# Optimization experiments

Measured on AMD Instinct MI355X. Metric: run time of the kernel, lower is better.

## Reference

```python
import jax, jax.numpy as jnp
import numpy as np

D = 1024
H = 16
HD = D // H


def setup_inputs() -> dict:
    key = jax.random.key(0)
    ks = jax.random.split(key, 9)
    s = 1.0 / np.sqrt(D)
    return {
        "x": jax.random.normal(ks[0], (2, 2048, D), dtype=jnp.float32),
        "Wq": jax.random.normal(ks[1], (D, D), dtype=jnp.float32) * s,
        "bq": jax.random.normal(ks[2], (D,), dtype=jnp.float32) * s,
        "Wk": jax.random.normal(ks[3], (D, D), dtype=jnp.float32) * s,
        "bk": jax.random.normal(ks[4], (D,), dtype=jnp.float32) * s,
        "Wv": jax.random.normal(ks[5], (D, D), dtype=jnp.float32) * s,
        "bv": jax.random.normal(ks[6], (D,), dtype=jnp.float32) * s,
        "Wo": jax.random.normal(ks[7], (D, D), dtype=jnp.float32) * s,
        "bo": jax.random.normal(ks[8], (D,), dtype=jnp.float32) * s,
    }


def reference(x, Wq, bq, Wk, bk, Wv, bv, Wo, bo):
    B, S, _ = x.shape
    # Linear projections (torch Linear: y = x @ W.T + b)
    q = x @ Wq.T + bq
    k = x @ Wk.T + bk
    v = x @ Wv.T + bv
    # split heads: [B, S, H, HD] -> [B, H, S, HD]
    q = q.reshape(B, S, H, HD).transpose(0, 2, 1, 3)
    k = k.reshape(B, S, H, HD).transpose(0, 2, 1, 3)
    v = v.reshape(B, S, H, HD).transpose(0, 2, 1, 3)
    scale = 1.0 / jnp.sqrt(jnp.float32(HD))
    scores = jnp.einsum("bhqd,bhkd->bhqk", q, k) * scale  # [B,H,S,S]
    attn = jax.nn.softmax(scores, axis=-1)
    ctx = jnp.einsum("bhqk,bhkd->bhqd", attn, v)  # [B,H,S,HD]
    ctx = ctx.transpose(0, 2, 1, 3).reshape(B, S, D)
    out = ctx @ Wo.T + bo
    return out, attn
```

## Files before the change

### kernel.cpp

```cpp
#include <hip/hip_runtime.h>

#define S_LEN 2048
#define NH 16
#define HDIM 64
#define DMODEL 1024
#define NTOK 4096

typedef __attribute__((ext_vector_type(8))) short bf16x8;
typedef __attribute__((ext_vector_type(4))) float f32x4;

__device__ __forceinline__ unsigned short f2bf(float f) {
  union { float f; unsigned int u; } a; a.f = f;
  unsigned int u = a.u;
  u += 0x7FFFu + ((u >> 16) & 1u);
  return (unsigned short)(u >> 16);
}

__device__ __forceinline__ void gld_lds16(const unsigned short* g, unsigned short* l) {
  auto gp = (const __attribute__((address_space(1))) unsigned short*)(g);
  auto lp = (__attribute__((address_space(3))) unsigned short*)(l);
  __builtin_amdgcn_global_load_lds(gp, lp, 16, 0, 0);
}

__global__ __launch_bounds__(256) void cvt_kernel(const float* __restrict__ s,
                                                  unsigned short* __restrict__ d, int n) {
  int i = (blockIdx.x * 256 + threadIdx.x) * 4;
  if (i >= n) return;
  float4 v = *(const float4*)(s + i);
  ushort4 o;
  o.x = f2bf(v.x); o.y = f2bf(v.y); o.z = f2bf(v.z); o.w = f2bf(v.w);
  *(ushort4*)(d + i) = o;
}

__device__ __forceinline__ void gemm_core_128(
    const unsigned short* __restrict__ A, const unsigned short* __restrict__ B,
    unsigned short* Al, unsigned short* Bl, int m0, int n0, int tid, f32x4 acc[4][4])
{
  const int lane = tid & 63;
  const int wm = ((tid >> 6) >> 1) * 64;
  const int wn = ((tid >> 6) & 1) * 64;
  const int l15 = lane & 15, quad = lane >> 4;
  const int row0 = tid >> 2, c8 = (tid & 3) * 8;
  for (int kk = 0; kk < DMODEL; kk += 32) {
    gld_lds16(A + (size_t)(m0 + row0) * DMODEL + kk + c8,      Al + tid * 8);
    gld_lds16(A + (size_t)(m0 + 64 + row0) * DMODEL + kk + c8, Al + (256 + tid) * 8);
    gld_lds16(B + (size_t)(n0 + row0) * DMODEL + kk + c8,      Bl + tid * 8);
    gld_lds16(B + (size_t)(n0 + 64 + row0) * DMODEL + kk + c8, Bl + (256 + tid) * 8);
    __syncthreads();
    bf16x8 af[4], bfr[4];
#pragma unroll
    for (int i = 0; i < 4; i++) {
      af[i]  = *(const bf16x8*)(Al + (wm + i * 16 + l15) * 32 + quad * 8);
      bfr[i] = *(const bf16x8*)(Bl + (wn + i * 16 + l15) * 32 + quad * 8);
    }
#pragma unroll
    for (int i = 0; i < 4; i++)
#pragma unroll
      for (int j = 0; j < 4; j++)
        acc[i][j] = __builtin_amdgcn_mfma_f32_16x16x32_bf16(af[i], bfr[j], acc[i][j], 0, 0, 0);
    __syncthreads();
  }
}

__global__ __launch_bounds__(256) void gemm_qkv(
    const unsigned short* __restrict__ xb,
    const unsigned short* __restrict__ wq, const unsigned short* __restrict__ wk,
    const unsigned short* __restrict__ wv,
    const float* __restrict__ bq, const float* __restrict__ bk, const float* __restrict__ bv,
    unsigned short* __restrict__ q_ws, unsigned short* __restrict__ k_ws,
    unsigned short* __restrict__ vT_ws)
{
  __shared__ unsigned short Al[128 * 32];
  __shared__ unsigned short Bl[128 * 32];
  const int which = blockIdx.z;
  const unsigned short* W = which == 0 ? wq : (which == 1 ? wk : wv);
  const float* bias = which == 0 ? bq : (which == 1 ? bk : bv);
  const int m0 = blockIdx.y * 128, n0 = blockIdx.x * 128;
  const int tid = threadIdx.x, lane = tid & 63;
  const int wm = ((tid >> 6) >> 1) * 64, wn = ((tid >> 6) & 1) * 64;
  const int l15 = lane & 15, quad = lane >> 4;
  f32x4 acc[4][4] = {};
  gemm_core_128(xb, W, Al, Bl, m0, n0, tid, acc);
  const float scale = (which == 0) ? 0.125f : 1.0f;
  unsigned short* qk_dst = (which == 0) ? q_ws : k_ws;
#pragma unroll
  for (int j = 0; j < 4; j++) {
    const int n = n0 + wn + j * 16 + l15;
    const float bb = bias[n];
    const int h = n >> 6, d = n & 63;
#pragma unroll
    for (int i = 0; i < 4; i++)
#pragma unroll
      for (int r = 0; r < 4; r++) {
        const int m = m0 + wm + i * 16 + quad * 4 + r;
        const int b = m >> 11, s = m & 2047;
        const unsigned short o = f2bf((acc[i][j][r] + bb) * scale);
        if (which == 2)
          vT_ws[((size_t)(b * NH + h) * HDIM + d) * S_LEN + s] = o;
        else
          qk_dst[((size_t)(b * NH + h) * S_LEN + s) * HDIM + d] = o;
      }
  }
}

__global__ __launch_bounds__(256, 8) void attn_fused(
    const unsigned short* __restrict__ q_ws, const unsigned short* __restrict__ k_ws,
    const unsigned short* __restrict__ vT_ws,
    float* __restrict__ attn_out, unsigned short* __restrict__ ctx_ws)
{
  __shared__ __align__(16) unsigned short p_lds[4][16 * 72];
  __shared__ float ls[4][16];
  const int tid = threadIdx.x, lane = tid & 63, w = tid >> 6;
  const int l15 = lane & 15, quad = lane >> 4;
  const int rowg = w >> 1, khalf = w & 1;
  const int bh = blockIdx.x >> 6, qt = blockIdx.x & 63;
  const int qr0 = qt * 32 + rowg * 16;
  const int kc0 = khalf * 1024;

  const unsigned short* qp = q_ws + ((size_t)bh * S_LEN + qr0 + l15) * HDIM + quad * 8;
  bf16x8 aq0 = *(const bf16x8*)qp;
  bf16x8 aq1 = *(const bf16x8*)(qp + 32);

  const unsigned short* kbh = k_ws + (size_t)bh * S_LEN * HDIM;
  const unsigned short* vbh = vT_ws + (size_t)bh * HDIM * S_LEN;

  float lsum = 0.f;
  for (int kc = kc0; kc < kc0 + 1024; kc += 64) {
#pragma unroll
    for (int t = 0; t < 4; t++) {
      const unsigned short* kb = kbh + (size_t)(kc + t * 16 + l15) * HDIM + quad * 8;
      bf16x8 b0 = *(const bf16x8*)kb;
      bf16x8 b1 = *(const bf16x8*)(kb + 32);
      f32x4 s = {0.f, 0.f, 0.f, 0.f};
      s = __builtin_amdgcn_mfma_f32_16x16x32_bf16(b0, aq0, s, 0, 0, 0);
      s = __builtin_amdgcn_mfma_f32_16x16x32_bf16(b1, aq1, s, 0, 0, 0);
      lsum += (__expf(s[0]) + __expf(s[1])) + (__expf(s[2]) + __expf(s[3]));
    }
  }
  float v = lsum;
  v += __shfl_xor(v, 16, 64);
  v += __shfl_xor(v, 32, 64);
  if (lane < 16) ls[w][lane] = v;
  __syncthreads();
  const float rinv = 1.0f / (v + ls[w ^ 1][l15]);

  f32x4 cacc[4] = {};
  float* abp = attn_out + ((size_t)bh * S_LEN + qr0 + l15) * S_LEN + quad * 4;
  unsigned short* plw = &p_lds[w][0];
  for (int kc = kc0; kc < kc0 + 1024; kc += 64) {
#pragma unroll
    for (int t = 0; t < 4; t++) {
      const unsigned short* kb = kbh + (size_t)(kc + t * 16 + l15) * HDIM + quad * 8;
      bf16x8 b0 = *(const bf16x8*)kb;
      bf16x8 b1 = *(const bf16x8*)(kb + 32);
      f32x4 s = {0.f, 0.f, 0.f, 0.f};
      s = __builtin_amdgcn_mfma_f32_16x16x32_bf16(b0, aq0, s, 0, 0, 0);
      s = __builtin_amdgcn_mfma_f32_16x16x32_bf16(b1, aq1, s, 0, 0, 0);
#pragma unroll
      for (int r = 0; r < 4; r++) s[r] = __expf(s[r]) * rinv;
      *(f32x4*)(abp + kc + t * 16) = s;
      ushort4 pk;
      pk.x = f2bf(s[0]); pk.y = f2bf(s[1]); pk.z = f2bf(s[2]); pk.w = f2bf(s[3]);
      *(ushort4*)(plw + l15 * 72 + t * 16 + quad * 4) = pk;
    }
    bf16x8 ap0 = *(const bf16x8*)(plw + l15 * 72 + quad * 8);
    bf16x8 ap1 = *(const bf16x8*)(plw + l15 * 72 + 32 + quad * 8);
#pragma unroll
    for (int dt = 0; dt < 4; dt++) {
      const unsigned short* vb = vbh + (size_t)(dt * 16 + l15) * S_LEN + kc + quad * 8;
      bf16x8 v0 = *(const bf16x8*)vb;
      bf16x8 v1 = *(const bf16x8*)(vb + 32);
      cacc[dt] = __builtin_amdgcn_mfma_f32_16x16x32_bf16(ap0, v0, cacc[dt], 0, 0, 0);
      cacc[dt] = __builtin_amdgcn_mfma_f32_16x16x32_bf16(ap1, v1, cacc[dt], 0, 0, 0);
    }
  }

  __syncthreads();
  float* cb = (float*)&p_lds[0][0];
  if (khalf) {
#pragma unroll
    for (int dt = 0; dt < 4; dt++)
      *(f32x4*)(cb + (rowg * 64 + lane) * 16 + dt * 4) = cacc[dt];
  }
  __syncthreads();
  if (!khalf) {
#pragma unroll
    for (int dt = 0; dt < 4; dt++)
      cacc[dt] += *(const f32x4*)(cb + (rowg * 64 + lane) * 16 + dt * 4);
    const int b = bh >> 4, h = bh & 15;
#pragma unroll
    for (int dt = 0; dt < 4; dt++)
#pragma unroll
      for (int r = 0; r < 4; r++) {
        const int s_ = qr0 + quad * 4 + r;
        const int d = dt * 16 + l15;
        ctx_ws[((size_t)(b * S_LEN + s_) * NH + h) * HDIM + d] = f2bf(cacc[dt][r]);
      }
  }
}

__global__ __launch_bounds__(256) void gemm_out(
    const unsigned short* __restrict__ ctx, const unsigned short* __restrict__ wo,
    const float* __restrict__ bo, float* __restrict__ out)
{
  __shared__ unsigned short Al[128 * 32];
  __shared__ unsigned short Bl[128 * 32];
  const int m0 = blockIdx.y * 128, n0 = blockIdx.x * 128;
  const int tid = threadIdx.x, lane = tid & 63;
  const int wm = ((tid >> 6) >> 1) * 64, wn = ((tid >> 6) & 1) * 64;
  const int l15 = lane & 15, quad = lane >> 4;
  f32x4 acc[4][4] = {};
  gemm_core_128(ctx, wo, Al, Bl, m0, n0, tid, acc);
#pragma unroll
  for (int j = 0; j < 4; j++) {
    const int n = n0 + wn + j * 16 + l15;
    const float bb = bo[n];
#pragma unroll
    for (int i = 0; i < 4; i++)
#pragma unroll
      for (int r = 0; r < 4; r++) {
        const int m = m0 + wm + i * 16 + quad * 4 + r;
        out[(size_t)m * DMODEL + n] = acc[i][j][r] + bb;
      }
  }
}

extern "C" void kernel_launch(void* const* d_in, const int* in_sizes, int n_in,
                              void* d_out, int out_size, void* d_ws, size_t ws_size,
                              hipStream_t stream) {
  const float* x  = (const float*)d_in[0];
  const float* Wq = (const float*)d_in[1];
  const float* bq = (const float*)d_in[2];
  const float* Wk = (const float*)d_in[3];
  const float* bk = (const float*)d_in[4];
  const float* Wv = (const float*)d_in[5];
  const float* bv = (const float*)d_in[6];
  const float* Wo = (const float*)d_in[7];
  const float* bo = (const float*)d_in[8];

  const size_t MB = 1u << 20;
  char* ws = (char*)d_ws;
  unsigned short* xb     = (unsigned short*)(ws);
  unsigned short* wqb    = (unsigned short*)(ws + 8 * MB);
  unsigned short* wkb    = (unsigned short*)(ws + 10 * MB);
  unsigned short* wvb    = (unsigned short*)(ws + 12 * MB);
  unsigned short* wob    = (unsigned short*)(ws + 14 * MB);
  unsigned short* q_ws   = (unsigned short*)(ws + 16 * MB);
  unsigned short* k_ws   = (unsigned short*)(ws + 24 * MB);
  unsigned short* vT_ws  = (unsigned short*)(ws + 32 * MB);
  unsigned short* ctx_ws = (unsigned short*)(ws + 40 * MB);

  float* out_ptr  = (float*)d_out;
  float* attn_ptr = (float*)d_out + 4194304;

  cvt_kernel<<<4096, 256, 0, stream>>>(x,  xb,  4194304);
  cvt_kernel<<<1024, 256, 0, stream>>>(Wq, wqb, 1048576);
  cvt_kernel<<<1024, 256, 0, stream>>>(Wk, wkb, 1048576);
  cvt_kernel<<<1024, 256, 0, stream>>>(Wv, wvb, 1048576);
  cvt_kernel<<<1024, 256, 0, stream>>>(Wo, wob, 1048576);

  gemm_qkv<<<dim3(8, 32, 3), 256, 0, stream>>>(xb, wqb, wkb, wvb, bq, bk, bv,
                                               q_ws, k_ws, vT_ws);
  attn_fused<<<2048, 256, 0, stream>>>(q_ws, k_ws, vT_ws, attn_ptr, ctx_ws);
  gemm_out<<<dim3(8, 32, 1), 256, 0, stream>>>(ctx_ws, wob, bo, out_ptr);
}
```

Before: 1.010 ms.

## Cache exp scores in LDS to avoid recomputing QK^T in attention

The attention kernel now computes QK^T and exp once per 16-row query tile, keeps the full 16x2048 row of exponentials in LDS, and reuses it for both the normalized attn store and the PV matmul. This removes the second QK^T pass and its K reloads. Work is split across 8 waves of 512-thread blocks, and attn is written with coalesced nontemporal row stores. The context is normalized after accumulation. The catch is about 132KB of LDS per block, which limits occupancy to one block per CU and puts more pressure on LDS bandwidth.

```diff
diff --git a/kernel.cpp b/kernel.cpp
--- a/kernel.cpp
+++ b/kernel.cpp
@@ -5,6 +5,7 @@
 #define HDIM 64
 #define DMODEL 1024
 #define NTOK 4096
+#define RSW 2060
 
 typedef __attribute__((ext_vector_type(8))) short bf16x8;
 typedef __attribute__((ext_vector_type(4))) float f32x4;
@@ -103,29 +104,27 @@
   }
 }
 
-__global__ __launch_bounds__(256, 8) void attn_fused(
+__global__ __launch_bounds__(512, 1) void attn_fused(
     const unsigned short* __restrict__ q_ws, const unsigned short* __restrict__ k_ws,
     const unsigned short* __restrict__ vT_ws,
     float* __restrict__ attn_out, unsigned short* __restrict__ ctx_ws)
 {
-  __shared__ __align__(16) unsigned short p_lds[4][16 * 72];
-  __shared__ float ls[4][16];
+  __shared__ float S_lds[16 * RSW];
+  __shared__ float ls[8][16];
   const int tid = threadIdx.x, lane = tid & 63, w = tid >> 6;
   const int l15 = lane & 15, quad = lane >> 4;
-  const int rowg = w >> 1, khalf = w & 1;
-  const int bh = blockIdx.x >> 6, qt = blockIdx.x & 63;
-  const int qr0 = qt * 32 + rowg * 16;
-  const int kc0 = khalf * 1024;
+  const int bh = blockIdx.x >> 7, qt = blockIdx.x & 127;
+  const int qr0 = qt * 16;
+  const int kc0 = w * 256;
 
   const unsigned short* qp = q_ws + ((size_t)bh * S_LEN + qr0 + l15) * HDIM + quad * 8;
-  bf16x8 aq0 = *(const bf16x8*)qp;
-  bf16x8 aq1 = *(const bf16x8*)(qp + 32);
-
+  const bf16x8 aq0 = *(const bf16x8*)qp;
+  const bf16x8 aq1 = *(const bf16x8*)(qp + 32);
   const unsigned short* kbh = k_ws + (size_t)bh * S_LEN * HDIM;
   const unsigned short* vbh = vT_ws + (size_t)bh * HDIM * S_LEN;
 
   float lsum = 0.f;
-  for (int kc = kc0; kc < kc0 + 1024; kc += 64) {
+  for (int kc = kc0; kc < kc0 + 256; kc += 64) {
 #pragma unroll
     for (int t = 0; t < 4; t++) {
       const unsigned short* kb = kbh + (size_t)(kc + t * 16 + l15) * HDIM + quad * 8;
@@ -134,69 +133,79 @@
       f32x4 s = {0.f, 0.f, 0.f, 0.f};
       s = __builtin_amdgcn_mfma_f32_16x16x32_bf16(b0, aq0, s, 0, 0, 0);
       s = __builtin_amdgcn_mfma_f32_16x16x32_bf16(b1, aq1, s, 0, 0, 0);
-      lsum += (__expf(s[0]) + __expf(s[1])) + (__expf(s[2]) + __expf(s[3]));
-    }
-  }
-  float v = lsum;
-  v += __shfl_xor(v, 16, 64);
-  v += __shfl_xor(v, 32, 64);
-  if (lane < 16) ls[w][lane] = v;
+      f32x4 e;
+#pragma unroll
+      for (int r = 0; r < 4; r++) e[r] = __expf(s[r]);
+      lsum += (e[0] + e[1]) + (e[2] + e[3]);
+      *(f32x4*)&S_lds[l15 * RSW + kc + t * 16 + quad * 4] = e;
+    }
+  }
+  {
+    float v = lsum;
+    v += __shfl_xor(v, 16, 64);
+    v += __shfl_xor(v, 32, 64);
+    if (lane < 16) ls[w][lane] = v;
+  }
   __syncthreads();
-  const float rinv = 1.0f / (v + ls[w ^ 1][l15]);
+
+  const int row0 = w * 2;
+  float t0 = 0.f, t1 = 0.f;
+#pragma unroll
+  for (int wv = 0; wv < 8; wv++) { t0 += ls[wv][row0]; t1 += ls[wv][row0 + 1]; }
+  const float rinv0 = 1.0f / t0, rinv1 = 1.0f / t1;
 
   f32x4 cacc[4] = {};
-  float* abp = attn_out + ((size_t)bh * S_LEN + qr0 + l15) * S_LEN + quad * 4;
-  unsigned short* plw = &p_lds[w][0];
-  for (int kc = kc0; kc < kc0 + 1024; kc += 64) {
-#pragma unroll
-    for (int t = 0; t < 4; t++) {
-      const unsigned short* kb = kbh + (size_t)(kc + t * 16 + l15) * HDIM + quad * 8;
-      bf16x8 b0 = *(const bf16x8*)kb;
-      bf16x8 b1 = *(const bf16x8*)(kb + 32);
-      f32x4 s = {0.f, 0.f, 0.f, 0.f};
-      s = __builtin_amdgcn_mfma_f32_16x16x32_bf16(b0, aq0, s, 0, 0, 0);
-      s = __builtin_amdgcn_mfma_f32_16x16x32_bf16(b1, aq1, s, 0, 0, 0);
-#pragma unroll
-      for (int r = 0; r < 4; r++) s[r] = __expf(s[r]) * rinv;
-      *(f32x4*)(abp + kc + t * 16) = s;
-      ushort4 pk;
-      pk.x = f2bf(s[0]); pk.y = f2bf(s[1]); pk.z = f2bf(s[2]); pk.w = f2bf(s[3]);
-      *(ushort4*)(plw + l15 * 72 + t * 16 + quad * 4) = pk;
-    }
-    bf16x8 ap0 = *(const bf16x8*)(plw + l15 * 72 + quad * 8);
-    bf16x8 ap1 = *(const bf16x8*)(plw + l15 * 72 + 32 + quad * 8);
+  for (int kk = 0; kk < 256; kk += 32) {
+    const int base = l15 * RSW + kc0 + kk + quad * 8;
+    f32x4 pa = *(const f32x4*)&S_lds[base];
+    f32x4 pb = *(const f32x4*)&S_lds[base + 4];
+    bf16x8 ap;
+#pragma unroll
+    for (int j = 0; j < 4; j++) {
+      ap[j]     = (short)f2bf(pa[j]);
+      ap[4 + j] = (short)f2bf(pb[j]);
+    }
 #pragma unroll
     for (int dt = 0; dt < 4; dt++) {
-      const unsigned short* vb = vbh + (size_t)(dt * 16 + l15) * S_LEN + kc + quad * 8;
+      const unsigned short* vb = vbh + (size_t)(dt * 16 + l15) * S_LEN + kc0 + kk + quad * 8;
       bf16x8 v0 = *(const bf16x8*)vb;
-      bf16x8 v1 = *(const bf16x8*)(vb + 32);
-      cacc[dt] = __builtin_amdgcn_mfma_f32_16x16x32_bf16(ap0, v0, cacc[dt], 0, 0, 0);
-      cacc[dt] = __builtin_amdgcn_mfma_f32_16x16x32_bf16(ap1, v1, cacc[dt], 0, 0, 0);
+      cacc[dt] = __builtin_amdgcn_mfma_f32_16x16x32_bf16(ap, v0, cacc[dt], 0, 0, 0);
+    }
+  }
+
+  {
+    float* g0 = attn_out + ((size_t)bh * S_LEN + qr0 + row0) * S_LEN;
+    float* g1 = g0 + S_LEN;
+#pragma unroll
+    for (int c = 0; c < 8; c++) {
+      f32x4 v0 = *(const f32x4*)&S_lds[row0 * RSW + c * 256 + lane * 4];
+      f32x4 v1 = *(const f32x4*)&S_lds[(row0 + 1) * RSW + c * 256 + lane * 4];
+#pragma unroll
+      for (int j = 0; j < 4; j++) { v0[j] *= rinv0; v1[j] *= rinv1; }
+      __builtin_nontemporal_store(v0, (f32x4*)(g0 + c * 256 + lane * 4));
+      __builtin_nontemporal_store(v1, (f32x4*)(g1 + c * 256 + lane * 4));
     }
   }
 
   __syncthreads();
-  float* cb = (float*)&p_lds[0][0];
-  if (khalf) {
-#pragma unroll
-    for (int dt = 0; dt < 4; dt++)
-      *(f32x4*)(cb + (rowg * 64 + lane) * 16 + dt * 4) = cacc[dt];
-  }
+
+  float* comb = &S_lds[0];
+#pragma unroll
+  for (int dt = 0; dt < 4; dt++)
+#pragma unroll
+    for (int r = 0; r < 4; r++)
+      comb[w * 1024 + (quad * 4 + r) * 64 + dt * 16 + l15] = cacc[dt][r];
   __syncthreads();
-  if (!khalf) {
-#pragma unroll
-    for (int dt = 0; dt < 4; dt++)
-      cacc[dt] += *(const f32x4*)(cb + (rowg * 64 + lane) * 16 + dt * 4);
-    const int b = bh >> 4, h = bh & 15;
-#pragma unroll
-    for (int dt = 0; dt < 4; dt++)
-#pragma unroll
-      for (int r = 0; r < 4; r++) {
-        const int s_ = qr0 + quad * 4 + r;
-        const int d = dt * 16 + l15;
-        ctx_ws[((size_t)(b * S_LEN + s_) * NH + h) * HDIM + d] = f2bf(cacc[dt][r]);
-      }
-  }
+
+  const int b = bh >> 4, h = bh & 15;
+  float c0 = 0.f, c1 = 0.f;
+#pragma unroll
+  for (int wv = 0; wv < 8; wv++) {
+    c0 += comb[wv * 1024 + row0 * 64 + lane];
+    c1 += comb[wv * 1024 + (row0 + 1) * 64 + lane];
+  }
+  ctx_ws[((size_t)(b * S_LEN + qr0 + row0) * NH + h) * HDIM + lane]     = f2bf(c0 * rinv0);
+  ctx_ws[((size_t)(b * S_LEN + qr0 + row0 + 1) * NH + h) * HDIM + lane] = f2bf(c1 * rinv1);
 }
 
 __global__ __launch_bounds__(256) void gemm_out(
@@ -261,6 +270,6 @@
 
   gemm_qkv<<<dim3(8, 32, 3), 256, 0, stream>>>(xb, wqb, wkb, wvb, bq, bk, bv,
                                                q_ws, k_ws, vT_ws);
-  attn_fused<<<2048, 256, 0, stream>>>(q_ws, k_ws, vT_ws, attn_ptr, ctx_ws);
+  attn_fused<<<4096, 512, 0, stream>>>(q_ws, k_ws, vT_ws, attn_ptr, ctx_ws);
   gemm_out<<<dim3(8, 32, 1), 256, 0, stream>>>(ctx_ws, wob, bo, out_ptr);
 }
```

Result: faster. 826.2 us (-18.2%).
